# Kernel optimization log

Hardware: AMD Instinct MI355X
Metric: run time of the kernel (lower is better)

## Reference

```python
import jax, jax.numpy as jnp
import numpy as np

NUM_EXPERT = 16
IN_FEAT = 1024
OUT_FEAT = 1024
BATCH = 8192


def setup_inputs() -> dict:
    key = jax.random.key(0)
    k_inp, k_gate, k_w = jax.random.split(key, 3)
    inp = jax.random.normal(k_inp, (BATCH, IN_FEAT), dtype=jnp.float32)
    gate = jax.random.randint(k_gate, (BATCH,), 0, NUM_EXPERT, dtype=jnp.int32)
    # nn.Linear default init: uniform(-1/sqrt(in_feat), 1/sqrt(in_feat))
    bound = 1.0 / np.sqrt(IN_FEAT)
    weight = jax.random.uniform(
        k_w, (NUM_EXPERT, OUT_FEAT, IN_FEAT), dtype=jnp.float32,
        minval=-bound, maxval=bound)
    return {"inp": inp, "gate": gate, "weight": weight}


def reference(inp, gate, weight):
    # o[t] = weight[gate[t]] @ inp[t]
    # Loop over the (small, fixed) expert axis via lax.scan; each step does a
    # dense [B, in] @ [in, out] GEMM and keeps rows routed to that expert.
    num_expert, out_feat, _ = weight.shape
    batch = inp.shape[0]

    def body(o, xs):
        i, w = xs  # w: [out_feat, in_feat]
        y = inp @ w.T  # [batch, out_feat]
        sel = (gate == i)[:, None]
        return jnp.where(sel, y, o), None

    o0 = jnp.zeros((batch, out_feat), dtype=inp.dtype)
    o, _ = jax.lax.scan(body, o0, (jnp.arange(num_expert), weight))
    return o
```

## Files before the change

### kernel.cpp

```cpp
#include <hip/hip_runtime.h>
#include <hip/hip_bf16.h>

#define NE    16
#define KDIM  1024
#define NDIM  1024
#define BATCH 8192
#define TM    128
#define TN    128
#define MAXT  96

typedef __attribute__((ext_vector_type(8))) short short8;
typedef __attribute__((ext_vector_type(4))) float floatx4;
typedef unsigned short ushort_t;

#define O_TG0  1024
#define O_TE   2048
#define O_TEND 3072
#define O_GIDX 4096
#define O_TOK  36864
#define O_PA   73728
#define WS_REQ 17113088

#define GLOAD_LDS(gp, lp) __builtin_amdgcn_global_load_lds( \
    (const __attribute__((address_space(1))) unsigned int*)(gp), \
    (__attribute__((address_space(3))) unsigned int*)(lp), 16, 0, 0)

__device__ __forceinline__ unsigned int pk2bf(float x, float y) {
    __hip_bfloat162 h = __float22bfloat162_rn(make_float2(x, y));
    unsigned int u;
    __builtin_memcpy(&u, &h, 4);
    return u;
}


__global__ __launch_bounds__(1024) void map_k(
        const int* __restrict__ gate, int* __restrict__ gidx,
        int* __restrict__ tg0, int* __restrict__ te, int* __restrict__ tend) {
    __shared__ int ccnt[128][NE];
    __shared__ int cbase[128][NE];
    __shared__ int ebase[NE];
    __shared__ int etot[NE];
    const int tid = threadIdx.x;
    const int wv = tid >> 6, ln = tid & 63;

    ((int*)ccnt)[tid] = 0;
    ((int*)ccnt)[tid + 1024] = 0;
    __syncthreads();

    int e[8], rk[8];
    #pragma unroll
    for (int i = 0; i < 8; ++i) {
        const int chunk = wv * 8 + i;
        const int t = chunk * 64 + ln;
        const int ei = gate[t];
        unsigned long long m = ~0ull;
        #pragma unroll
        for (int b = 0; b < 4; ++b) {
            unsigned long long bb = __ballot(((ei >> b) & 1) != 0);
            m &= ((ei >> b) & 1) ? bb : ~bb;
        }
        const unsigned int lo = (unsigned int)m;
        const unsigned int hi = (unsigned int)(m >> 32);
        const int r = __builtin_amdgcn_mbcnt_hi(
            hi, __builtin_amdgcn_mbcnt_lo(lo, 0));
        if (r == 0) ccnt[chunk][ei] = __popcll(m);
        e[i] = ei; rk[i] = r;
    }
    __syncthreads();

    if (tid < NE) {
        int s = 0;
        for (int c = 0; c < 128; ++c) { cbase[c][tid] = s; s += ccnt[c][tid]; }
        etot[tid] = s;
    }
    __syncthreads();

    if (tid == 0) {
        int o = 0, nt = 0;
        for (int j = 0; j < NE; ++j) {
            ebase[j] = o;
            int c = etot[j];
            for (int rr = 0; rr < c; rr += TM) {
                int r0 = (rr + TM <= c) ? rr : (c > TM ? c - TM : 0);
                tg0[nt] = o + r0; te[nt] = j; tend[nt] = o + c; ++nt;
            }
            o += c;
        }
        for (; nt < MAXT; ++nt) { tg0[nt] = 0; te[nt] = 0; tend[nt] = 0; }
    }
    __syncthreads();

    #pragma unroll
    for (int i = 0; i < 8; ++i) {
        const int chunk = wv * 8 + i;
        const int t = chunk * 64 + ln;
        gidx[t] = ebase[e[i]] + cbase[chunk][e[i]] + rk[i];
    }
}

__global__ __launch_bounds__(256, 8) void gather_k(
        const float* __restrict__ inp, const int* __restrict__ gidx,
        ushort_t* __restrict__ pA, int* __restrict__ tok) {
    const int b = blockIdx.x, tid = threadIdx.x;
    const int col = (tid & 127) * 8;
    const int half = tid >> 7;
    int g[2]; float4 v0[2], v1[2];
    #pragma unroll
    for (int p = 0; p < 2; ++p) {
        int t = b * 4 + p * 2 + half;
        g[p] = gidx[t];
        v0[p] = *(const float4*)&inp[(size_t)t * KDIM + col];
        v1[p] = *(const float4*)&inp[(size_t)t * KDIM + col + 4];
    }
    #pragma unroll
    for (int p = 0; p < 2; ++p) {
        uint4 u = make_uint4(pk2bf(v0[p].x, v0[p].y), pk2bf(v0[p].z, v0[p].w),
                             pk2bf(v1[p].x, v1[p].y), pk2bf(v1[p].z, v1[p].w));
        *(uint4*)&pA[(size_t)g[p] * KDIM + col] = u;
        if (col == 0) tok[g[p]] = b * 4 + p * 2 + half;
    }
}

__global__ __launch_bounds__(256, 3) void moe_gemm9_k(
        const ushort_t* __restrict__ pA, const float* __restrict__ wgt,
        const int* __restrict__ tg0, const int* __restrict__ teArr,
        const int* __restrict__ tend, const int* __restrict__ tok,
        float* __restrict__ out) {
    const int y   = blockIdx.y;
    const int g0  = tg0[y];
    const int end = tend[y];
    if (g0 >= end) return;
    const int e    = teArr[y];
    const int out0 = blockIdx.x * TN;

    __shared__ ushort_t As[TM][64];
    __shared__ ushort_t Bs[TN][64];
    __shared__ int tok_s[TM];

    const int tid = threadIdx.x;
    if (tid < TM) tok_s[tid] = tok[g0 + tid];

    const int wave = tid >> 6, lane = tid & 63;
    const int wm = (wave >> 1) * 64;
    const int wn = (wave & 1) * 64;
    const int quad = lane >> 4, l16 = lane & 15;

    const ushort_t* Ab = pA + (size_t)g0 * KDIM;
    const float*    Bw = wgt + ((size_t)e * NDIM + out0) * KDIM;

    floatx4 acc[4][4] = {};
    const int slotw = wave * 64 + lane;

    for (int k0 = 0; k0 < KDIM; k0 += 64) {
        float4 bv[4][2];
        #pragma unroll
        for (int i = 0; i < 4; ++i) {
            int slot = i * 256 + slotw;
            int row = slot >> 3;
            int kc = (slot & 7) ^ (row & 7);
            const float* src = Bw + (size_t)row * KDIM + k0 + kc * 8;
            bv[i][0] = *(const float4*)src;
            bv[i][1] = *(const float4*)(src + 4);
        }
        #pragma unroll
        for (int i = 0; i < 4; ++i) {
            int slot = i * 256 + slotw;
            int row = slot >> 3;
            int kc = (slot & 7) ^ (row & 7);
            GLOAD_LDS(Ab + (size_t)row * KDIM + k0 + kc * 8,
                      (ushort_t*)As + (size_t)(i * 256 + wave * 64) * 8);
        }
        #pragma unroll
        for (int i = 0; i < 4; ++i) {
            int slot = i * 256 + slotw;
            uint4 u = make_uint4(pk2bf(bv[i][0].x, bv[i][0].y),
                                 pk2bf(bv[i][0].z, bv[i][0].w),
                                 pk2bf(bv[i][1].x, bv[i][1].y),
                                 pk2bf(bv[i][1].z, bv[i][1].w));
            *(uint4*)((ushort_t*)Bs + (size_t)slot * 8) = u;
        }
        __syncthreads();
        #pragma unroll
        for (int s = 0; s < 2; ++s) {
            short8 a[4], b[4];
            #pragma unroll
            for (int i = 0; i < 4; ++i) {
                int r = wm + i * 16 + l16;
                a[i] = *(const short8*)&As[r][((s * 4 + quad) ^ (r & 7)) * 8];
            }
            #pragma unroll
            for (int j = 0; j < 4; ++j) {
                int r = wn + j * 16 + l16;
                b[j] = *(const short8*)&Bs[r][((s * 4 + quad) ^ (r & 7)) * 8];
            }
            #pragma unroll
            for (int mi = 0; mi < 4; ++mi)
                #pragma unroll
                for (int nj = 0; nj < 4; ++nj)
                    acc[mi][nj] = __builtin_amdgcn_mfma_f32_16x16x32_bf16(
                        a[mi], b[nj], acc[mi][nj], 0, 0, 0);
        }
        __syncthreads();
    }

    #pragma unroll
    for (int mi = 0; mi < 4; ++mi) {
        #pragma unroll
        for (int r = 0; r < 4; ++r) {
            int lrow = wm + mi * 16 + quad * 4 + r;
            if (g0 + lrow < end) {
                int t = tok_s[lrow];
                float* orow = out + (size_t)t * NDIM + out0 + wn + l16;
                #pragma unroll
                for (int nj = 0; nj < 4; ++nj)
                    orow[nj * 16] = acc[mi][nj][r];
            }
        }
    }
}

#define LDW 20
__global__ void zero_k(int* cnt) {
    if (threadIdx.x < NE) cnt[threadIdx.x] = 0;
}

__global__ void bin_tokens_k(const int* __restrict__ gate, int* cnt, int* idx) {
    int t = blockIdx.x * blockDim.x + threadIdx.x;
    if (t < BATCH) {
        int e = gate[t];
        int p = atomicAdd(&cnt[e], 1);
        idx[e * BATCH + p] = t;
    }
}

__global__ __launch_bounds__(256) void moe_gemm_k(
        const float* __restrict__ inp, const float* __restrict__ wgt,
        const int* __restrict__ cnt, const int* __restrict__ idx,
        float* __restrict__ out) {
    const int e = blockIdx.z;
    const int n_e = cnt[e];
    const int row0 = blockIdx.y * TM;
    if (row0 >= n_e) return;
    const int out0 = blockIdx.x * 128;
    __shared__ unsigned int As[TM * LDW];
    __shared__ unsigned int Bs[TM * LDW];
    __shared__ int tok_s[TM];
    const int tid = threadIdx.x;
    if (tid < TM) {
        int g = row0 + tid;
        tok_s[tid] = (g < n_e) ? idx[e * BATCH + g] : -1;
    }
    const int wave = tid >> 6, lane = tid & 63;
    const int wm = (wave >> 1) * 64, wn = (wave & 1) * 64;
    const int quad = lane >> 4, l16 = lane & 15;
    floatx4 acc[4][4] = {};
    const int cg = (tid & 7) * 4;
    const int rbase = tid >> 3;
    const float* wbase = wgt + (size_t)e * KDIM * NDIM;
    for (int k0 = 0; k0 < KDIM; k0 += 32) {
        __syncthreads();
        #pragma unroll
        for (int p = 0; p < 4; ++p) {
            int row = p * 32 + rbase;
            int t = tok_s[row];
            float4 va = make_float4(0.f, 0.f, 0.f, 0.f);
            if (t >= 0) va = *(const float4*)&inp[(size_t)t * KDIM + k0 + cg];
            As[row * LDW + (cg >> 1)]     = pk2bf(va.x, va.y);
            As[row * LDW + (cg >> 1) + 1] = pk2bf(va.z, va.w);
            float4 vb = *(const float4*)&wbase[(size_t)(out0 + row) * KDIM + k0 + cg];
            Bs[row * LDW + (cg >> 1)]     = pk2bf(vb.x, vb.y);
            Bs[row * LDW + (cg >> 1) + 1] = pk2bf(vb.z, vb.w);
        }
        __syncthreads();
        short8 a[4], b[4];
        #pragma unroll
        for (int i = 0; i < 4; ++i)
            a[i] = *(const short8*)&As[(wm + i * 16 + l16) * LDW + quad * 4];
        #pragma unroll
        for (int i = 0; i < 4; ++i)
            b[i] = *(const short8*)&Bs[(wn + i * 16 + l16) * LDW + quad * 4];
        #pragma unroll
        for (int mi = 0; mi < 4; ++mi)
            #pragma unroll
            for (int ni = 0; ni < 4; ++ni)
                acc[mi][ni] = __builtin_amdgcn_mfma_f32_16x16x32_bf16(
                    a[mi], b[ni], acc[mi][ni], 0, 0, 0);
    }
    #pragma unroll
    for (int mi = 0; mi < 4; ++mi) {
        #pragma unroll
        for (int r = 0; r < 4; ++r) {
            int lrow = wm + mi * 16 + quad * 4 + r;
            int t = tok_s[lrow];
            if (t >= 0) {
                float* orow = out + (size_t)t * NDIM + out0 + wn + l16;
                #pragma unroll
                for (int ni = 0; ni < 4; ++ni)
                    orow[ni * 16] = acc[mi][ni][r];
            }
        }
    }
}

extern "C" void kernel_launch(void* const* d_in, const int* in_sizes, int n_in,
                              void* d_out, int out_size, void* d_ws, size_t ws_size,
                              hipStream_t stream) {
    const float* inp  = (const float*)d_in[0];
    const int*   gate = (const int*)d_in[1];
    const float* wgt  = (const float*)d_in[2];
    float*       out  = (float*)d_out;
    char* w = (char*)d_ws;

    if (ws_size >= WS_REQ) {
        int* tg0  = (int*)(w + O_TG0);
        int* te   = (int*)(w + O_TE);
        int* tend = (int*)(w + O_TEND);
        int* gidx = (int*)(w + O_GIDX);
        int* tok  = (int*)(w + O_TOK);
        ushort_t* pA = (ushort_t*)(w + O_PA);

        map_k<<<1, 1024, 0, stream>>>(gate, gidx, tg0, te, tend);
        gather_k<<<2048, 256, 0, stream>>>(inp, gidx, pA, tok);
        dim3 grid(NDIM / TN, MAXT, 1);
        moe_gemm9_k<<<grid, 256, 0, stream>>>(pA, wgt, tg0, te, tend, tok, out);
    } else {
        int* cnt = (int*)d_ws;
        int* idx = cnt + NE;
        zero_k<<<1, 64, 0, stream>>>(cnt);
        bin_tokens_k<<<BATCH / 256, 256, 0, stream>>>(gate, cnt, idx);
        dim3 grid(NDIM / 128, BATCH / TM, NE);
        moe_gemm_k<<<grid, 256, 0, stream>>>(inp, wgt, cnt, idx, out);
    }
}
```

Baseline: 183.6 us.

## Reshape grouped GEMM tiles to 256x64 with per-tile lower bound masking

Measured after the change: 174.0 us. 5.3% less time.

```diff
diff --git a/kernel.cpp b/kernel.cpp
--- a/kernel.cpp
+++ b/kernel.cpp
@@ -5,9 +5,9 @@
 #define KDIM  1024
 #define NDIM  1024
 #define BATCH 8192
-#define TM    128
-#define TN    128
-#define MAXT  96
+#define TM    256
+#define TN    64
+#define MAXT  48
 
 typedef __attribute__((ext_vector_type(8))) short short8;
 typedef __attribute__((ext_vector_type(4))) float floatx4;
@@ -16,6 +16,7 @@
 #define O_TG0  1024
 #define O_TE   2048
 #define O_TEND 3072
+#define O_TLO  3584
 #define O_GIDX 4096
 #define O_TOK  36864
 #define O_PA   73728
@@ -35,7 +36,8 @@
 
 __global__ __launch_bounds__(1024) void map_k(
         const int* __restrict__ gate, int* __restrict__ gidx,
-        int* __restrict__ tg0, int* __restrict__ te, int* __restrict__ tend) {
+        int* __restrict__ tg0, int* __restrict__ te, int* __restrict__ tend,
+        int* __restrict__ tlo) {
     __shared__ int ccnt[128][NE];
     __shared__ int cbase[128][NE];
     __shared__ int ebase[NE];
@@ -81,12 +83,14 @@
             ebase[j] = o;
             int c = etot[j];
             for (int rr = 0; rr < c; rr += TM) {
-                int r0 = (rr + TM <= c) ? rr : (c > TM ? c - TM : 0);
-                tg0[nt] = o + r0; te[nt] = j; tend[nt] = o + c; ++nt;
+                int g0;
+                if (c >= TM) g0 = o + ((rr + TM <= c) ? rr : c - TM);
+                else         g0 = (o <= BATCH - TM) ? o : BATCH - TM;
+                tg0[nt] = g0; tlo[nt] = o; te[nt] = j; tend[nt] = o + c; ++nt;
             }
             o += c;
         }
-        for (; nt < MAXT; ++nt) { tg0[nt] = 0; te[nt] = 0; tend[nt] = 0; }
+        for (; nt < MAXT; ++nt) { tg0[nt] = 0; te[nt] = 0; tend[nt] = 0; tlo[nt] = 0; }
     }
     __syncthreads();
 
@@ -121,15 +125,16 @@
     }
 }
 
-__global__ __launch_bounds__(256, 3) void moe_gemm9_k(
+__global__ __launch_bounds__(256, 3) void moe_gemm11_k(
         const ushort_t* __restrict__ pA, const float* __restrict__ wgt,
         const int* __restrict__ tg0, const int* __restrict__ teArr,
-        const int* __restrict__ tend, const int* __restrict__ tok,
-        float* __restrict__ out) {
+        const int* __restrict__ tend, const int* __restrict__ tloArr,
+        const int* __restrict__ tok, float* __restrict__ out) {
     const int y   = blockIdx.y;
     const int g0  = tg0[y];
     const int end = tend[y];
     if (g0 >= end) return;
+    const int lo   = tloArr[y];
     const int e    = teArr[y];
     const int out0 = blockIdx.x * TN;
 
@@ -138,24 +143,22 @@
     __shared__ int tok_s[TM];
 
     const int tid = threadIdx.x;
-    if (tid < TM) tok_s[tid] = tok[g0 + tid];
+    tok_s[tid] = tok[g0 + tid];
 
     const int wave = tid >> 6, lane = tid & 63;
-    const int wm = (wave >> 1) * 64;
-    const int wn = (wave & 1) * 64;
+    const int wm = wave * 64;
     const int quad = lane >> 4, l16 = lane & 15;
 
     const ushort_t* Ab = pA + (size_t)g0 * KDIM;
     const float*    Bw = wgt + ((size_t)e * NDIM + out0) * KDIM;
 
     floatx4 acc[4][4] = {};
-    const int slotw = wave * 64 + lane;
 
     for (int k0 = 0; k0 < KDIM; k0 += 64) {
-        float4 bv[4][2];
-        #pragma unroll
-        for (int i = 0; i < 4; ++i) {
-            int slot = i * 256 + slotw;
+        float4 bv[2][2];
+        #pragma unroll
+        for (int i = 0; i < 2; ++i) {
+            int slot = i * 256 + tid;
             int row = slot >> 3;
             int kc = (slot & 7) ^ (row & 7);
             const float* src = Bw + (size_t)row * KDIM + k0 + kc * 8;
@@ -163,16 +166,16 @@
             bv[i][1] = *(const float4*)(src + 4);
         }
         #pragma unroll
-        for (int i = 0; i < 4; ++i) {
-            int slot = i * 256 + slotw;
+        for (int i = 0; i < 8; ++i) {
+            int slot = i * 256 + tid;
             int row = slot >> 3;
             int kc = (slot & 7) ^ (row & 7);
             GLOAD_LDS(Ab + (size_t)row * KDIM + k0 + kc * 8,
                       (ushort_t*)As + (size_t)(i * 256 + wave * 64) * 8);
         }
         #pragma unroll
-        for (int i = 0; i < 4; ++i) {
-            int slot = i * 256 + slotw;
+        for (int i = 0; i < 2; ++i) {
+            int slot = i * 256 + tid;
             uint4 u = make_uint4(pk2bf(bv[i][0].x, bv[i][0].y),
                                  pk2bf(bv[i][0].z, bv[i][0].w),
                                  pk2bf(bv[i][1].x, bv[i][1].y),
@@ -190,7 +193,7 @@
             }
             #pragma unroll
             for (int j = 0; j < 4; ++j) {
-                int r = wn + j * 16 + l16;
+                int r = j * 16 + l16;
                 b[j] = *(const short8*)&Bs[r][((s * 4 + quad) ^ (r & 7)) * 8];
             }
             #pragma unroll
@@ -208,9 +211,10 @@
         #pragma unroll
         for (int r = 0; r < 4; ++r) {
             int lrow = wm + mi * 16 + quad * 4 + r;
-            if (g0 + lrow < end) {
+            int gi = g0 + lrow;
+            if (gi >= lo && gi < end) {
                 int t = tok_s[lrow];
-                float* orow = out + (size_t)t * NDIM + out0 + wn + l16;
+                float* orow = out + (size_t)t * NDIM + out0 + l16;
                 #pragma unroll
                 for (int nj = 0; nj < 4; ++nj)
                     orow[nj * 16] = acc[mi][nj][r];
@@ -220,6 +224,7 @@
 }
 
 #define LDW 20
+#define TMF 128
 __global__ void zero_k(int* cnt) {
     if (threadIdx.x < NE) cnt[threadIdx.x] = 0;
 }
@@ -239,14 +244,14 @@
         float* __restrict__ out) {
     const int e = blockIdx.z;
     const int n_e = cnt[e];
-    const int row0 = blockIdx.y * TM;
+    const int row0 = blockIdx.y * TMF;
     if (row0 >= n_e) return;
     const int out0 = blockIdx.x * 128;
-    __shared__ unsigned int As[TM * LDW];
-    __shared__ unsigned int Bs[TM * LDW];
-    __shared__ int tok_s[TM];
+    __shared__ unsigned int As[TMF * LDW];
+    __shared__ unsigned int Bs[TMF * LDW];
+    __shared__ int tok_s[TMF];
     const int tid = threadIdx.x;
-    if (tid < TM) {
+    if (tid < TMF) {
         int g = row0 + tid;
         tok_s[tid] = (g < n_e) ? idx[e * BATCH + g] : -1;
     }
@@ -315,20 +320,22 @@
         int* tg0  = (int*)(w + O_TG0);
         int* te   = (int*)(w + O_TE);
         int* tend = (int*)(w + O_TEND);
+        int* tlo  = (int*)(w + O_TLO);
         int* gidx = (int*)(w + O_GIDX);
         int* tok  = (int*)(w + O_TOK);
         ushort_t* pA = (ushort_t*)(w + O_PA);
 
-        map_k<<<1, 1024, 0, stream>>>(gate, gidx, tg0, te, tend);
+        map_k<<<1, 1024, 0, stream>>>(gate, gidx, tg0, te, tend, tlo);
         gather_k<<<2048, 256, 0, stream>>>(inp, gidx, pA, tok);
         dim3 grid(NDIM / TN, MAXT, 1);
-        moe_gemm9_k<<<grid, 256, 0, stream>>>(pA, wgt, tg0, te, tend, tok, out);
+        moe_gemm11_k<<<grid, 256, 0, stream>>>(pA, wgt, tg0, te, tend, tlo,
+                                               tok, out);
     } else {
         int* cnt = (int*)d_ws;
         int* idx = cnt + NE;
         zero_k<<<1, 64, 0, stream>>>(cnt);
         bin_tokens_k<<<BATCH / 256, 256, 0, stream>>>(gate, cnt, idx);
-        dim3 grid(NDIM / 128, BATCH / TM, NE);
+        dim3 grid(NDIM / 128, BATCH / TMF, NE);
         moe_gemm_k<<<grid, 256, 0, stream>>>(inp, wgt, cnt, idx, out);
     }
 }
```
